# Kernel tuning notes

Hardware: AMD Instinct MI355X
Metric: run time of the kernel (lower is better)

Reference implementation:

```python
import jax, jax.numpy as jnp
import numpy as np

N = 100000   # num_nodes_total
E = 1600000  # num edges (avg degree 16)
ES = 30000   # scored triples
R = 16       # num_relations
D = 128      # cfg.dim


def setup_inputs() -> dict:
    key = jax.random.key(0)
    ks = jax.random.split(key, 10)
    x0 = 0.01 * jax.random.normal(ks[0], (N, D), dtype=jnp.float32)  # Embedding init std=0.01
    # GCNConv lin: Glorot init, no bias in lin; separate zero bias added post-aggregation
    glorot = np.sqrt(6.0 / (D + D)).astype(np.float32)
    W1 = jax.random.uniform(ks[1], (D, D), jnp.float32, -glorot, glorot)
    b1 = jnp.zeros((D,), jnp.float32)
    W2 = jax.random.uniform(ks[2], (D, D), jnp.float32, -glorot, glorot)
    b2 = jnp.zeros((D,), jnp.float32)
    rel_W = jax.random.uniform(ks[3], (R, D, D), jnp.float32, -glorot, glorot)  # xavier_uniform
    edge_index = jax.random.randint(ks[4], (2, E), 0, N)
    rel_ids = jax.random.randint(ks[5], (ES,), 0, R)
    head = jax.random.randint(ks[6], (ES,), 0, N)
    tail = jax.random.randint(ks[7], (ES,), 0, N)
    return {"x0": x0, "W1": W1, "b1": b1, "W2": W2, "b2": b2,
            "rel_W": rel_W, "edge_index": edge_index, "rel_ids": rel_ids,
            "head": head, "tail": tail}


def _gcn_conv(x, W, b, src, dst, norm):
    # GCNConv(add_self_loops=False, normalize=True): out = scatter(norm * (xW)[src] -> dst) + b
    h = x @ W                           # (N, D)
    msg = h[src] * norm[:, None]        # (E, D)
    return jax.ops.segment_sum(msg, dst, num_segments=x.shape[0]) + b


def reference(x0, W1, b1, W2, b2, rel_W, edge_index, rel_ids, head, tail):
    src, dst = edge_index[0], edge_index[1]
    n = x0.shape[0]
    # symmetric gcn_norm without self-loops: deg over targets, norm = d^-1/2[src]*d^-1/2[dst]
    deg = jax.ops.segment_sum(jnp.ones_like(src, dtype=x0.dtype), dst, num_segments=n)
    dinv = jnp.where(deg > 0, 1.0 / jnp.sqrt(jnp.maximum(deg, 1.0)), 0.0)
    norm = dinv[src] * dinv[dst]
    # encode (eval mode: dropout is identity)
    x = jax.nn.relu(_gcn_conv(x0, W1, b1, src, dst, norm))
    z = _gcn_conv(x, W2, b2, src, dst, norm)
    # score_logits_all_rel: z[head]^T W[rel] z[tail]
    scores = jnp.einsum('ed,edf,ef->e', z[head], rel_W[rel_ids], z[tail])
    return scores
```

## Files before the change

kernel.cpp:

```cpp
#include <hip/hip_runtime.h>
#include <hip/hip_bf16.h>

#define TD 128
#define WS 136
#define SC_T 8
#define BKT_SH 7
#define NBLK 256

typedef __attribute__((ext_vector_type(8))) short bf16x8;
typedef __attribute__((ext_vector_type(4))) float f32x4;

static __device__ __forceinline__ unsigned short f2bf(float f) {
    unsigned int u = __float_as_uint(f);
    u += 0x7fffu + ((u >> 16) & 1u);
    return (unsigned short)(u >> 16);
}
static __device__ __forceinline__ float bf2f(unsigned short h) {
    return __uint_as_float((unsigned int)h << 16);
}


__global__ __launch_bounds__(256) void kc_hist(const int* __restrict__ ei, int* __restrict__ bh,
                                               const int* __restrict__ rel, int* __restrict__ rbh,
                                               const float* __restrict__ W1, const float* __restrict__ W2,
                                               unsigned short* __restrict__ Wt,
                                               unsigned char* __restrict__ need, int N_,
                                               int E_, int ES_, int NB, int chunk, int rchunk) {
    __shared__ int lh[1024];
    __shared__ int rh[16];
    int t = threadIdx.x, blk = blockIdx.x;
    if (blk >= NBLK + 64) {
        int i4 = (blk - NBLK - 64) * 256 + t;
        if (i4 * 16 < N_) ((uint4*)need)[i4] = make_uint4(0u, 0u, 0u, 0u);
        return;
    }
    if (blk >= NBLK) {
        int idx = (blk - NBLK) * 256 + t;
        int k = idx >> 7, n = idx & 127;
        Wt[n * 128 + k] = f2bf(W1[idx]);
        Wt[16384 + n * 128 + k] = f2bf(W2[idx]);
        return;
    }
    for (int j = t; j < NB; j += 256) lh[j] = 0;
    if (t < 16) rh[t] = 0;
    __syncthreads();
    int e0 = blk * chunk, e1 = min(E_, e0 + chunk);
    for (int e = e0 + t; e < e1; e += 256)
        atomicAdd(&lh[ei[E_ + e] >> BKT_SH], 1);
    int r0 = blk * rchunk, r1 = min(ES_, r0 + rchunk);
    for (int e = r0 + t; e < r1; e += 256)
        atomicAdd(&rh[rel[e]], 1);
    __syncthreads();
    for (int j = t; j < NB; j += 256) bh[(size_t)j * NBLK + blk] = lh[j];
    if (t < 16) rbh[(size_t)t * NBLK + blk] = rh[t];
}

__global__ __launch_bounds__(64) void kc_scanA(int* __restrict__ bh, int* __restrict__ tot, int NB) {
    int b = blockIdx.x, l = threadIdx.x;
    int* row = bh + (size_t)b * NBLK;
    int run = 0;
#pragma unroll
    for (int g = 0; g < NBLK / 64; ++g) {
        int v = row[g * 64 + l];
        int x = v;
#pragma unroll
        for (int off = 1; off < 64; off <<= 1) {
            int y = __shfl_up(x, off);
            if (l >= off) x += y;
        }
        row[g * 64 + l] = run + x - v;
        run += __shfl(x, 63);
    }
    if (l == 0) tot[b] = run;
}

__global__ __launch_bounds__(256) void kc_scanB(const int* __restrict__ tot, int* __restrict__ boff,
                                                int NB, int* __restrict__ rowptrN,
                                                const int* __restrict__ rbh, int* __restrict__ roff,
                                                int* __restrict__ chunkoff, int* __restrict__ cursor, int nr) {
    __shared__ int wsum[4];
    __shared__ int rseg[16][17];
    int t = threadIdx.x;
    {
        int rl = t & 15, seg = t >> 4;
        const int per = NBLK / 16;
        int ps = 0;
        for (int k = 0; k < per; ++k) ps += rbh[(size_t)rl * NBLK + seg * per + k];
        rseg[rl][seg] = ps;
    }
    int base = t * 4;
    int a0 = (base     < NB) ? tot[base]     : 0;
    int a1 = (base + 1 < NB) ? tot[base + 1] : 0;
    int a2 = (base + 2 < NB) ? tot[base + 2] : 0;
    int a3 = (base + 3 < NB) ? tot[base + 3] : 0;
    int s1 = a0 + a1, s2 = s1 + a2, tt = s2 + a3;
    int lane = t & 63, wv = t >> 6;
    int x = tt;
#pragma unroll
    for (int off = 1; off < 64; off <<= 1) {
        int y = __shfl_up(x, off);
        if (lane >= off) x += y;
    }
    if (lane == 63) wsum[wv] = x;
    __syncthreads();
    int woff = 0;
    for (int w = 0; w < wv; ++w) woff += wsum[w];
    int excl = woff + x - tt;
    if (base     < NB) boff[base]     = excl;
    if (base + 1 < NB) boff[base + 1] = excl + a0;
    if (base + 2 < NB) boff[base + 2] = excl + s1;
    if (base + 3 < NB) boff[base + 3] = excl + s2;
    if (t == 255) { boff[NB] = woff + x; *rowptrN = woff + x; }
    if (t == 0) {
        int run = 0, crun = 0;
        for (int r = 0; r < nr; ++r) {
            int rc = 0;
#pragma unroll
            for (int sg = 0; sg < 16; ++sg) rc += rseg[r][sg];
            roff[r] = run; chunkoff[r] = crun; cursor[r] = run;
            run += rc; crun += (rc + SC_T - 1) / SC_T;
        }
        roff[nr] = run; chunkoff[nr] = crun;
    }
}

__global__ __launch_bounds__(256) void kc_scat(const int* __restrict__ ei, const int* __restrict__ bh,
                                               const int* __restrict__ boff, int* __restrict__ ebuf,
                                               int E_, int NB, int chunk,
                                               const int* __restrict__ rel, int* __restrict__ cursor,
                                               int* __restrict__ eidx, const int* __restrict__ head,
                                               const int* __restrict__ tail, unsigned char* __restrict__ need,
                                               int ES_) {
    __shared__ int lh[1024];
    __shared__ int lbase[16];
    int t = threadIdx.x, blk = blockIdx.x;
    if (blk >= NBLK) {
        int b2 = blk - NBLK;
        if (t < 16) lh[t] = 0;
        __syncthreads();
        int r[4], lr[4];
#pragma unroll
        for (int i = 0; i < 4; ++i) {
            int e = b2 * 1024 + i * 256 + t;
            if (e < ES_) {
                r[i] = rel[e];
                lr[i] = atomicAdd(&lh[r[i]], 1);
                need[head[e]] = 1;
                need[tail[e]] = 1;
            } else r[i] = -1;
        }
        __syncthreads();
        if (t < 16) lbase[t] = lh[t] ? atomicAdd(&cursor[t], lh[t]) : 0;
        __syncthreads();
#pragma unroll
        for (int i = 0; i < 4; ++i)
            if (r[i] >= 0) eidx[lbase[r[i]] + lr[i]] = b2 * 1024 + i * 256 + t;
        return;
    }
    for (int j = t; j < NB; j += 256) lh[j] = 0;
    __syncthreads();
    int e0 = blk * chunk, e1 = min(E_, e0 + chunk);
    for (int e = e0 + t; e < e1; e += 256) {
        int s = ei[e];
        int d = ei[E_ + e];
        int b = d >> BKT_SH;
        int lr = atomicAdd(&lh[b], 1);
        int slot = boff[b] + bh[(size_t)b * NBLK + blk] + lr;
        ebuf[slot] = (s << BKT_SH) | (d & ((1 << BKT_SH) - 1));
    }
}

__global__ __launch_bounds__(256) void kc_build(const int* __restrict__ ebuf, const int* __restrict__ boff,
                                                int* __restrict__ rowptr, float* __restrict__ dinv,
                                                int* __restrict__ esrc, int n) {
    __shared__ int hist[128], excl[128], cur[128];
    __shared__ int w0;
    int b = blockIdx.x, t = threadIdx.x;
    int node0 = b << BKT_SH;
    int s = boff[b], e = boff[b + 1];
    if (t < 128) { hist[t] = 0; cur[t] = 0; }
    __syncthreads();
    for (int i = s + t; i < e; i += 256)
        atomicAdd(&hist[ebuf[i] & 127], 1);
    __syncthreads();
    int v = (t < 128) ? hist[t] : 0;
    int lane = t & 63, wv = t >> 6;
    int x = v;
#pragma unroll
    for (int off = 1; off < 64; off <<= 1) {
        int y = __shfl_up(x, off);
        if (lane >= off) x += y;
    }
    if (t == 63) w0 = x;
    __syncthreads();
    if (t < 128) {
        int ex = x - v + (wv == 1 ? w0 : 0);
        excl[t] = ex;
        int node = node0 + t;
        if (node < n) {
            rowptr[node] = s + ex;
            dinv[node] = (v > 0) ? 1.0f / sqrtf((float)v) : 0.0f;
        }
    }
    __syncthreads();
    for (int i = s + t; i < e; i += 256) {
        int p = ebuf[i];
        int loc = p & 127;
        int lr = atomicAdd(&cur[loc], 1);
        esrc[s + excl[loc] + lr] = p >> BKT_SH;
    }
}

__global__ __launch_bounds__(256, 4) void k_gemm(const void* __restrict__ Xv,
                                                 const unsigned short* __restrict__ Wth,
                                                 const float* __restrict__ scale,
                                                 unsigned char* __restrict__ out8,
                                                 float* __restrict__ scOut,
                                                 int nrows, int ibf16) {
    __shared__ __align__(16) unsigned short Wl[128 * WS];
    const int t = threadIdx.x;
    const int w = t >> 6;
    const int lane = t & 63;
    const int l15 = lane & 15;
    const int quad = lane >> 4;
    const int rbase = blockIdx.x * 64 + w * 16;
    const int arow = rbase + l15;
    const bool avalid = arow < nrows;

    bf16x8 ah[4];
    const bf16x8 zero8 = {0, 0, 0, 0, 0, 0, 0, 0};
    if (ibf16) {
        const unsigned short* Xb = (const unsigned short*)Xv;
#pragma unroll
        for (int kc = 0; kc < 4; ++kc)
            ah[kc] = avalid ? *(const bf16x8*)(Xb + (size_t)arow * TD + kc * 32 + quad * 8) : zero8;
    } else {
        const float* X = (const float*)Xv;
        float4 xa[4][2];
#pragma unroll
        for (int kc = 0; kc < 4; ++kc) {
            const float* src = X + (size_t)arow * TD + kc * 32 + quad * 8;
            xa[kc][0] = avalid ? *(const float4*)src       : make_float4(0.f, 0.f, 0.f, 0.f);
            xa[kc][1] = avalid ? *(const float4*)(src + 4) : make_float4(0.f, 0.f, 0.f, 0.f);
        }
#pragma unroll
        for (int kc = 0; kc < 4; ++kc)
#pragma unroll
            for (int j = 0; j < 8; ++j) {
                float v = (j < 4) ? ((const float*)&xa[kc][0])[j] : ((const float*)&xa[kc][1])[j - 4];
                ah[kc][j] = (short)f2bf(v);
            }
    }

    {
        const uint4* gh = (const uint4*)Wth;
#pragma unroll
        for (int it = 0; it < 8; ++it) {
            int idx = t + it * 256;
            int n = idx >> 4, kg = idx & 15;
            uint4 vh = gh[idx];
            *(uint4*)&Wl[n * WS + kg * 8] = vh;
        }
    }
    __syncthreads();

    f32x4 acc[8];
#pragma unroll
    for (int b = 0; b < 8; ++b) acc[b] = (f32x4){0.f, 0.f, 0.f, 0.f};

#pragma unroll
    for (int kc = 0; kc < 4; ++kc) {
        const int koff = kc * 32 + quad * 8;
#pragma unroll
        for (int b = 0; b < 8; ++b) {
            bf16x8 bh = *(const bf16x8*)&Wl[(b * 16 + l15) * WS + koff];
            acc[b] = __builtin_amdgcn_mfma_f32_16x16x32_bf16(ah[kc], bh, acc[b], 0, 0, 0);
        }
    }

    __syncthreads();

    {
        unsigned char* lds8 = (unsigned char*)&Wl[0];
        const int grow = rbase + quad * 4;
        float4 s4 = make_float4(0.f, 0.f, 0.f, 0.f);
        if (grow < nrows) s4 = *(const float4*)&scale[grow];
        float rm[4];
#pragma unroll
        for (int j = 0; j < 4; ++j) {
            float sj = ((const float*)&s4)[j];
            float mx = 0.f;
#pragma unroll
            for (int b = 0; b < 8; ++b) {
                acc[b][j] *= sj;
                mx = fmaxf(mx, fabsf(acc[b][j]));
            }
            rm[j] = mx;
        }
#pragma unroll
        for (int m_ = 1; m_ < 16; m_ <<= 1)
#pragma unroll
            for (int j = 0; j < 4; ++j) rm[j] = fmaxf(rm[j], __shfl_xor(rm[j], m_));
        float inv[4];
#pragma unroll
        for (int j = 0; j < 4; ++j) inv[j] = rm[j] > 0.f ? 127.f / rm[j] : 0.f;
#pragma unroll
        for (int j = 0; j < 4; ++j) {
            int lrow = w * 16 + quad * 4 + j;
#pragma unroll
            for (int b = 0; b < 8; ++b) {
                int q = (int)rintf(acc[b][j] * inv[j]);
                lds8[lrow * 128 + b * 16 + l15] = (unsigned char)(signed char)q;
            }
        }
        if (l15 == 0 && grow < nrows)
            *(float4*)&scOut[grow] = make_float4(rm[0] * (1.f / 127.f), rm[1] * (1.f / 127.f),
                                                 rm[2] * (1.f / 127.f), rm[3] * (1.f / 127.f));
    }
    __syncthreads();
    {
        const unsigned int* lds32 = (const unsigned int*)&Wl[0];
        unsigned int* g32 = (unsigned int*)out8;
#pragma unroll
        for (int k = 0; k < 8; ++k) {
            int idx = t + k * 256;
            int row = blockIdx.x * 64 + (idx >> 5);
            if (row < nrows) g32[(size_t)blockIdx.x * 2048 + idx] = lds32[idx];
        }
    }
}

#define ACCI8(p, u, s) \
    p##0 = fmaf(s, (float)(signed char)(u.x      ), p##0); \
    p##1 = fmaf(s, (float)(signed char)(u.x >>  8), p##1); \
    p##2 = fmaf(s, (float)(signed char)(u.x >> 16), p##2); \
    p##3 = fmaf(s, (float)(signed char)(u.x >> 24), p##3); \
    p##4 = fmaf(s, (float)(signed char)(u.y      ), p##4); \
    p##5 = fmaf(s, (float)(signed char)(u.y >>  8), p##5); \
    p##6 = fmaf(s, (float)(signed char)(u.y >> 16), p##6); \
    p##7 = fmaf(s, (float)(signed char)(u.y >> 24), p##7);

__global__ __launch_bounds__(256) void k_agg(const unsigned char* __restrict__ hs8, const float* __restrict__ sc,
                                             const int* __restrict__ rowptr, const int* __restrict__ esrc,
                                             const float* __restrict__ dinv, const float* __restrict__ bias,
                                             void* __restrict__ outv, int n, int relu, int obf16,
                                             const unsigned char* __restrict__ need) {
    int node = blockIdx.x * 16 + (threadIdx.x >> 4);
    int lane = threadIdx.x & 15;
    if (node >= n) return;
    if (need && !need[node]) return;
    int s = rowptr[node], e = rowptr[node + 1];
    const uint2* h8 = (const uint2*)hs8;
    float a0 = 0.f, a1 = 0.f, a2 = 0.f, a3 = 0.f, a4 = 0.f, a5 = 0.f, a6 = 0.f, a7 = 0.f;
    float c0 = 0.f, c1 = 0.f, c2 = 0.f, c3 = 0.f, c4 = 0.f, c5 = 0.f, c6 = 0.f, c7 = 0.f;
    int i = s;
    for (; i + 4 <= e; i += 4) {
        int s0 = esrc[i], s1 = esrc[i + 1], s2 = esrc[i + 2], s3 = esrc[i + 3];
        uint2 u0 = h8[(size_t)s0 * 16 + lane];
        uint2 u1 = h8[(size_t)s1 * 16 + lane];
        uint2 u2 = h8[(size_t)s2 * 16 + lane];
        uint2 u3 = h8[(size_t)s3 * 16 + lane];
        float f0 = sc[s0], f1 = sc[s1], f2 = sc[s2], f3 = sc[s3];
        ACCI8(a, u0, f0)
        ACCI8(c, u1, f1)
        ACCI8(a, u2, f2)
        ACCI8(c, u3, f3)
    }
    for (; i < e; ++i) {
        int s0 = esrc[i];
        uint2 u = h8[(size_t)s0 * 16 + lane];
        float f = sc[s0];
        ACCI8(a, u, f)
    }
    a0 += c0; a1 += c1; a2 += c2; a3 += c3;
    a4 += c4; a5 += c5; a6 += c6; a7 += c7;
    float di = dinv[node];
    float4 b0 = ((const float4*)bias)[lane * 2];
    float4 b1 = ((const float4*)bias)[lane * 2 + 1];
    float o0 = fmaf(di, a0, b0.x);
    float o1 = fmaf(di, a1, b0.y);
    float o2 = fmaf(di, a2, b0.z);
    float o3 = fmaf(di, a3, b0.w);
    float o4 = fmaf(di, a4, b1.x);
    float o5 = fmaf(di, a5, b1.y);
    float o6 = fmaf(di, a6, b1.z);
    float o7 = fmaf(di, a7, b1.w);
    if (relu) {
        o0 = fmaxf(o0, 0.f); o1 = fmaxf(o1, 0.f); o2 = fmaxf(o2, 0.f); o3 = fmaxf(o3, 0.f);
        o4 = fmaxf(o4, 0.f); o5 = fmaxf(o5, 0.f); o6 = fmaxf(o6, 0.f); o7 = fmaxf(o7, 0.f);
    }
    if (obf16) {
        unsigned int p0 = (unsigned int)f2bf(o0) | ((unsigned int)f2bf(o1) << 16);
        unsigned int p1 = (unsigned int)f2bf(o2) | ((unsigned int)f2bf(o3) << 16);
        unsigned int p2 = (unsigned int)f2bf(o4) | ((unsigned int)f2bf(o5) << 16);
        unsigned int p3 = (unsigned int)f2bf(o6) | ((unsigned int)f2bf(o7) << 16);
        ((uint4*)outv)[(size_t)node * 16 + lane] = make_uint4(p0, p1, p2, p3);
    } else {
        ((float4*)outv)[(size_t)node * 32 + lane * 2]     = make_float4(o0, o1, o2, o3);
        ((float4*)outv)[(size_t)node * 32 + lane * 2 + 1] = make_float4(o4, o5, o6, o7);
    }
}

__global__ __launch_bounds__(256) void k_score_r(const float* __restrict__ z, const float* __restrict__ relW,
                                                 const int* __restrict__ eidx, const int* __restrict__ head,
                                                 const int* __restrict__ tail, const int* __restrict__ roff,
                                                 const int* __restrict__ chunkoff, float* __restrict__ out,
                                                 int R_, int cpb) {
    __shared__ __align__(16) float Wl[TD * TD];
    __shared__ __align__(16) float zhL[SC_T * TD];
    __shared__ __align__(16) float ztL[SC_T * TD];
    __shared__ int eids[SC_T];
    __shared__ int co[17], ro[17];
    __shared__ float red[4][SC_T];
    const int t = threadIdx.x;
    if (t < 17 && t <= R_) { co[t] = chunkoff[t]; ro[t] = roff[t]; }
    __syncthreads();
    const int nch = co[R_];
    int b = blockIdx.x * cpb;
    const int bend = min(nch, b + cpb);
    int r = 0, rprev = -1;
    for (; b < bend; ++b) {
        while (co[r + 1] <= b) ++r;
        const int base = ro[r] + (b - co[r]) * SC_T;
        const int nt = min(SC_T, ro[r + 1] - base);
        if (t < SC_T) eids[t] = (t < nt) ? eidx[base + t] : -1;
        const bool newW = (r != rprev);
        rprev = r;
        __syncthreads();
        {
            int tt = t >> 5, c4 = t & 31;
            float4 vh = make_float4(0.f, 0.f, 0.f, 0.f), vt = vh;
            int e = eids[tt];
            if (e >= 0) {
                vh = ((const float4*)(z + (size_t)head[e] * TD))[c4];
                vt = ((const float4*)(z + (size_t)tail[e] * TD))[c4];
            }
            ((float4*)(zhL + tt * TD))[c4] = vh;
            ((float4*)(ztL + tt * TD))[c4] = vt;
        }
        if (newW) {
            const float4* W4 = (const float4*)(relW + (size_t)r * TD * TD);
            float4* Wl4 = (float4*)Wl;
#pragma unroll
            for (int i = 0; i < 16; ++i) Wl4[t + i * 256] = W4[t + i * 256];
        }
        __syncthreads();

        const int c  = (t & 31) * 4;
        const int i0 = (t >> 5) * 16;
        float4 acc[SC_T];
#pragma unroll
        for (int u = 0; u < SC_T; ++u) acc[u] = make_float4(0.f, 0.f, 0.f, 0.f);
#pragma unroll 4
        for (int i = i0; i < i0 + 16; ++i) {
            float4 wv = *(const float4*)&Wl[i * TD + c];
#pragma unroll
            for (int u = 0; u < SC_T; ++u) {
                float h = zhL[u * TD + i];
                acc[u].x = fmaf(h, wv.x, acc[u].x);
                acc[u].y = fmaf(h, wv.y, acc[u].y);
                acc[u].z = fmaf(h, wv.z, acc[u].z);
                acc[u].w = fmaf(h, wv.w, acc[u].w);
            }
        }
        float pth[SC_T];
#pragma unroll
        for (int u = 0; u < SC_T; ++u) {
            float4 z4 = *(const float4*)&ztL[u * TD + c];
            pth[u] = acc[u].x * z4.x + acc[u].y * z4.y + acc[u].z * z4.z + acc[u].w * z4.w;
        }
#pragma unroll
        for (int off = 32; off > 0; off >>= 1)
#pragma unroll
            for (int u = 0; u < SC_T; ++u) pth[u] += __shfl_down(pth[u], off);
        if ((t & 63) == 0) {
            int wv = t >> 6;
#pragma unroll
            for (int u = 0; u < SC_T; ++u) red[wv][u] = pth[u];
        }
        __syncthreads();
        if (t < SC_T) {
            int e = eids[t];
            if (e >= 0) out[e] = red[0][t] + red[1][t] + red[2][t] + red[3][t];
        }
    }
}

extern "C" void kernel_launch(void* const* d_in, const int* in_sizes, int n_in,
                              void* d_out, int out_size, void* d_ws, size_t ws_size,
                              hipStream_t stream) {
    const float* x0   = (const float*)d_in[0];
    const float* W1   = (const float*)d_in[1];
    const float* b1   = (const float*)d_in[2];
    const float* W2   = (const float*)d_in[3];
    const float* b2   = (const float*)d_in[4];
    const float* relW = (const float*)d_in[5];
    const int*   ei   = (const int*)d_in[6];
    const int*   rel  = (const int*)d_in[7];
    const int*   head = (const int*)d_in[8];
    const int*   tail = (const int*)d_in[9];
    float* outp = (float*)d_out;

    const int N_  = in_sizes[0] / TD;
    const int E_  = in_sizes[6] / 2;
    const int ES_ = in_sizes[7];
    const int R_  = in_sizes[5] / (TD * TD);
    const int ntiles64 = (N_ + 63) / 64;
    const int NB    = (N_ + (1 << BKT_SH) - 1) >> BKT_SH;
    const int chunk  = (E_ + NBLK - 1) / NBLK;
    const int rchunk = (ES_ + NBLK - 1) / NBLK;
    const int nzb    = (N_ + 4095) / 4096;
    const int nbuck  = (ES_ + 1023) / 1024;
    const int maxch  = (ES_ + SC_T - 1) / SC_T + R_;
    const int sgrid  = maxch < 512 ? maxch : 512;
    const int cpb    = (maxch + sgrid - 1) / sgrid;

    char* p = (char*)d_ws;
    auto alloc = [&](size_t bytes) { char* r = p; p += (bytes + 255) & ~(size_t)255; return r; };
    float*          dinv   = (float*)         alloc((size_t)N_ * 4);
    int*            rowptr = (int*)           alloc(((size_t)N_ + 1) * 4);
    int*            bh     = (int*)           alloc((size_t)NB * NBLK * 4);
    int*            rbh    = (int*)           alloc((size_t)16 * NBLK * 4);
    int*            tot    = (int*)           alloc((size_t)NB * 4);
    int*            boff   = (int*)           alloc(((size_t)NB + 1) * 4);
    int*            esrc   = (int*)           alloc((size_t)E_ * 4);
    unsigned short* Wt     = (unsigned short*)alloc((size_t)2 * 16384 * 2);
    int*            roff   = (int*)           alloc(((size_t)R_ + 1) * 4);
    int*            chkoff = (int*)           alloc(((size_t)R_ + 1) * 4);
    int*            cursor = (int*)           alloc((size_t)R_ * 4);
    int*            eidx   = (int*)           alloc((size_t)ES_ * 4);
    unsigned char*  need   = (unsigned char*) alloc((size_t)N_ + 16);
    unsigned char*  bufA   = (unsigned char*) alloc((size_t)N_ * TD);
    float*          sc     = (float*)         alloc((size_t)N_ * 4);
    float*          bufB   = (float*)         alloc((size_t)N_ * TD * 4);
    int*            ebuf   = (int*)bufA;

    kc_hist <<<NBLK + 64 + nzb, 256, 0, stream>>>(ei, bh, rel, rbh, W1, W2, Wt, need, N_,
                                                  E_, ES_, NB, chunk, rchunk);
    kc_scanA<<<NB, 64, 0, stream>>>(bh, tot, NB);
    kc_scanB<<<1, 256, 0, stream>>>(tot, boff, NB, rowptr + N_, rbh, roff, chkoff, cursor, R_);
    kc_scat <<<NBLK + nbuck, 256, 0, stream>>>(ei, bh, boff, ebuf, E_, NB, chunk,
                                               rel, cursor, eidx, head, tail, need, ES_);
    kc_build<<<NB, 256, 0, stream>>>(ebuf, boff, rowptr, dinv, esrc, N_);

    k_gemm<<<ntiles64, 256, 0, stream>>>(x0, Wt, dinv, bufA, sc, N_, 0);
    k_agg <<<(N_ + 15) / 16, 256, 0, stream>>>(bufA, sc, rowptr, esrc, dinv, b1, bufB, N_, 1, 1, (const unsigned char*)nullptr);
    k_gemm<<<ntiles64, 256, 0, stream>>>(bufB, Wt + 16384, dinv, bufA, sc, N_, 1);
    k_agg <<<(N_ + 15) / 16, 256, 0, stream>>>(bufA, sc, rowptr, esrc, dinv, b2, bufB, N_, 0, 0, need);

    k_score_r<<<sgrid, 256, 0, stream>>>(bufB, relW, eidx, head, tail,
                                         roff, chkoff, outp, R_, cpb);
}
```

Before: 286.2 us.

## Unroll aggregation gathers to 8 and prefetch next score chunk into registers

The neighbor aggregation loop now issues eight independent row gathers per iteration, spread over four accumulator sets, with 2-wide and 1-wide tail loops. This raises memory-level parallelism on the latency-bound int8 gathers at the cost of more registers. The scoring kernel now loads the next chunk's edge ids and head/tail embedding rows into registers while the current chunk computes. It also restages the relation matrix only after the current chunk finishes, so one barrier per chunk is dropped and global gather latency overlaps compute.

```diff
diff --git a/kernel.cpp b/kernel.cpp
--- a/kernel.cpp
+++ b/kernel.cpp
@@ -353,20 +353,40 @@
     const uint2* h8 = (const uint2*)hs8;
     float a0 = 0.f, a1 = 0.f, a2 = 0.f, a3 = 0.f, a4 = 0.f, a5 = 0.f, a6 = 0.f, a7 = 0.f;
     float c0 = 0.f, c1 = 0.f, c2 = 0.f, c3 = 0.f, c4 = 0.f, c5 = 0.f, c6 = 0.f, c7 = 0.f;
+    float d0 = 0.f, d1 = 0.f, d2 = 0.f, d3 = 0.f, d4 = 0.f, d5 = 0.f, d6 = 0.f, d7 = 0.f;
+    float g0 = 0.f, g1 = 0.f, g2 = 0.f, g3 = 0.f, g4 = 0.f, g5 = 0.f, g6 = 0.f, g7 = 0.f;
     int i = s;
-    for (; i + 4 <= e; i += 4) {
-        int s0 = esrc[i], s1 = esrc[i + 1], s2 = esrc[i + 2], s3 = esrc[i + 3];
+    for (; i + 8 <= e; i += 8) {
+        int s0 = esrc[i],     s1 = esrc[i + 1], s2 = esrc[i + 2], s3 = esrc[i + 3];
+        int s4 = esrc[i + 4], s5 = esrc[i + 5], s6 = esrc[i + 6], s7 = esrc[i + 7];
         uint2 u0 = h8[(size_t)s0 * 16 + lane];
         uint2 u1 = h8[(size_t)s1 * 16 + lane];
         uint2 u2 = h8[(size_t)s2 * 16 + lane];
         uint2 u3 = h8[(size_t)s3 * 16 + lane];
+        uint2 u4 = h8[(size_t)s4 * 16 + lane];
+        uint2 u5 = h8[(size_t)s5 * 16 + lane];
+        uint2 u6 = h8[(size_t)s6 * 16 + lane];
+        uint2 u7 = h8[(size_t)s7 * 16 + lane];
         float f0 = sc[s0], f1 = sc[s1], f2 = sc[s2], f3 = sc[s3];
+        float f4 = sc[s4], f5 = sc[s5], f6 = sc[s6], f7 = sc[s7];
         ACCI8(a, u0, f0)
         ACCI8(c, u1, f1)
-        ACCI8(a, u2, f2)
-        ACCI8(c, u3, f3)
-    }
-    for (; i < e; ++i) {
+        ACCI8(d, u2, f2)
+        ACCI8(g, u3, f3)
+        ACCI8(a, u4, f4)
+        ACCI8(c, u5, f5)
+        ACCI8(d, u6, f6)
+        ACCI8(g, u7, f7)
+    }
+    for (; i + 2 <= e; i += 2) {
+        int s0 = esrc[i], s1 = esrc[i + 1];
+        uint2 u0 = h8[(size_t)s0 * 16 + lane];
+        uint2 u1 = h8[(size_t)s1 * 16 + lane];
+        float f0 = sc[s0], f1 = sc[s1];
+        ACCI8(a, u0, f0)
+        ACCI8(c, u1, f1)
+    }
+    if (i < e) {
         int s0 = esrc[i];
         uint2 u = h8[(size_t)s0 * 16 + lane];
         float f = sc[s0];
@@ -374,6 +394,10 @@
     }
     a0 += c0; a1 += c1; a2 += c2; a3 += c3;
     a4 += c4; a5 += c5; a6 += c6; a7 += c7;
+    d0 += g0; d1 += g1; d2 += g2; d3 += g3;
+    d4 += g4; d5 += g5; d6 += g6; d7 += g7;
+    a0 += d0; a1 += d1; a2 += d2; a3 += d3;
+    a4 += d4; a5 += d5; a6 += d6; a7 += d7;
     float di = dinv[node];
     float4 b0 = ((const float4*)bias)[lane * 2];
     float4 b1 = ((const float4*)bias)[lane * 2 + 1];
@@ -416,38 +440,47 @@
     if (t < 17 && t <= R_) { co[t] = chunkoff[t]; ro[t] = roff[t]; }
     __syncthreads();
     const int nch = co[R_];
-    int b = blockIdx.x * cpb;
-    const int bend = min(nch, b + cpb);
-    int r = 0, rprev = -1;
-    for (; b < bend; ++b) {
-        while (co[r + 1] <= b) ++r;
-        const int base = ro[r] + (b - co[r]) * SC_T;
-        const int nt = min(SC_T, ro[r + 1] - base);
-        if (t < SC_T) eids[t] = (t < nt) ? eidx[base + t] : -1;
-        const bool newW = (r != rprev);
-        rprev = r;
+    int b0 = (int)blockIdx.x * cpb;
+    const int bend = min(nch, b0 + cpb);
+    if (b0 >= bend) return;
+    const int tt = t >> 5, c4 = t & 31;
+    const int c  = (t & 31) * 4;
+    const int i0 = (t >> 5) * 16;
+
+    auto stage_W = [&](int rr) {
+        const float4* W4 = (const float4*)(relW + (size_t)rr * TD * TD);
+        float4* Wl4 = (float4*)Wl;
+#pragma unroll
+        for (int i = 0; i < 16; ++i) Wl4[t + i * 256] = W4[t + i * 256];
+    };
+    int eid_n;
+    float4 vh_n, vt_n;
+    auto pf = [&](int b, int rr) {
+        int base = ro[rr] + (b - co[rr]) * SC_T;
+        int nt2 = min(SC_T, ro[rr + 1] - base);
+        eid_n = (t < nt2) ? eidx[base + t] : -1;
+        int e = (tt < nt2) ? eidx[base + tt] : -1;
+        vh_n = make_float4(0.f, 0.f, 0.f, 0.f); vt_n = vh_n;
+        if (e >= 0) {
+            vh_n = ((const float4*)(z + (size_t)head[e] * TD))[c4];
+            vt_n = ((const float4*)(z + (size_t)tail[e] * TD))[c4];
+        }
+    };
+
+    int r = 0;
+    while (co[r + 1] <= b0) ++r;
+    stage_W(r);
+    pf(b0, r);
+    for (int b = b0; b < bend; ++b) {
+        if (t < SC_T) eids[t] = eid_n;
+        ((float4*)(zhL + tt * TD))[c4] = vh_n;
+        ((float4*)(ztL + tt * TD))[c4] = vt_n;
         __syncthreads();
-        {
-            int tt = t >> 5, c4 = t & 31;
-            float4 vh = make_float4(0.f, 0.f, 0.f, 0.f), vt = vh;
-            int e = eids[tt];
-            if (e >= 0) {
-                vh = ((const float4*)(z + (size_t)head[e] * TD))[c4];
-                vt = ((const float4*)(z + (size_t)tail[e] * TD))[c4];
-            }
-            ((float4*)(zhL + tt * TD))[c4] = vh;
-            ((float4*)(ztL + tt * TD))[c4] = vt;
-        }
-        if (newW) {
-            const float4* W4 = (const float4*)(relW + (size_t)r * TD * TD);
-            float4* Wl4 = (float4*)Wl;
-#pragma unroll
-            for (int i = 0; i < 16; ++i) Wl4[t + i * 256] = W4[t + i * 256];
-        }
-        __syncthreads();
-
-        const int c  = (t & 31) * 4;
-        const int i0 = (t >> 5) * 16;
+        int rn = r;
+        const bool havenext = (b + 1 < bend);
+        if (havenext) { while (co[rn + 1] <= b + 1) ++rn; }
+        if (havenext && rn == r) pf(b + 1, rn);
+
         float4 acc[SC_T];
 #pragma unroll
         for (int u = 0; u < SC_T; ++u) acc[u] = make_float4(0.f, 0.f, 0.f, 0.f);
@@ -483,6 +516,11 @@
             int e = eids[t];
             if (e >= 0) out[e] = red[0][t] + red[1][t] + red[2][t] + red[3][t];
         }
+        if (havenext && rn != r) {
+            stage_W(rn);
+            pf(b + 1, rn);
+        }
+        r = rn;
     }
 }
 
```

Result: slower. 299.8 us (+4.7%).
